# Optimization experiments

Measured on AMD Instinct MI355X. Metric: run time of the kernel, lower is better.

## Reference

```python
import jax, jax.numpy as jnp
import numpy as np

B, T, E, HH, V = 64, 128, 256, 256, 50000  # HH = hidden_size // 2 per LTC level
DT = 1.0


def setup_inputs() -> dict:
    key = jax.random.key(0)
    ks = jax.random.split(key, 12)
    s_in = 1.0 / np.sqrt(E)
    s_rec = 1.0 / np.sqrt(HH)
    tokens = jax.random.randint(ks[0], (B, T), 0, V, dtype=jnp.int32)
    emb = jax.random.normal(ks[1], (V, E), jnp.float32) * 0.02
    W_in0 = jax.random.normal(ks[2], (HH, E), jnp.float32) * s_in
    W_rec0 = jax.random.normal(ks[3], (HH, HH), jnp.float32) * s_rec
    b0 = jnp.zeros((HH,), jnp.float32)
    tau0 = jax.random.uniform(ks[4], (HH,), jnp.float32)
    # NCP sparsity mask: keep prob = 1 - sparsity_level = 0.5
    mask0 = (jax.random.uniform(ks[5], (HH, HH)) > 0.5).astype(jnp.float32)
    W_in1 = jax.random.normal(ks[6], (HH, HH), jnp.float32) * s_rec
    W_rec1 = jax.random.normal(ks[7], (HH, HH), jnp.float32) * s_rec
    b1 = jnp.zeros((HH,), jnp.float32)
    tau1 = jax.random.uniform(ks[8], (HH,), jnp.float32)
    mask1 = (jax.random.uniform(ks[9], (HH, HH)) > 0.5).astype(jnp.float32)
    return {"tokens": tokens, "emb": emb,
            "W_in0": W_in0, "W_rec0": W_rec0, "b0": b0, "tau0": tau0, "mask0": mask0,
            "W_in1": W_in1, "W_rec1": W_rec1, "b1": b1, "tau1": tau1, "mask1": mask1}


def _ltc_scan(x_seq, W_in, W_rec, mask, b, tau_raw):
    """LTC Euler integration over time. x_seq: [B, T, D] -> [B, T, H]."""
    tau = jax.nn.softplus(tau_raw) + 0.1        # positive time constants [H]
    Wr = W_rec * mask                            # NCP sparse recurrent weights
    x_proj = jnp.einsum('btd,hd->bth', x_seq, W_in) + b  # precompute input drive
    h0 = jnp.zeros((x_seq.shape[0], W_rec.shape[0]), x_seq.dtype)

    def step(h, xp_t):
        pre = xp_t + h @ Wr.T
        h_new = h + DT * ((-h + jnp.tanh(pre)) / tau)
        return h_new, h_new

    _, hs = jax.lax.scan(step, h0, jnp.swapaxes(x_proj, 0, 1))  # [T, B, H]
    return jnp.swapaxes(hs, 0, 1)


def reference(tokens, emb, W_in0, W_rec0, b0, tau0, mask0,
              W_in1, W_rec1, b1, tau1, mask1):
    x = emb[tokens]                                   # [B, T, E]
    h0_seq = _ltc_scan(x, W_in0, W_rec0, mask0, b0, tau0)      # level 0: [B, T, HH]
    h1_seq = _ltc_scan(h0_seq, W_in1, W_rec1, mask1, b1, tau1)  # level 1: [B, T, HH]
    return jnp.concatenate([h0_seq, h1_seq], axis=-1)  # [B, T, 2*HH] = hidden_size
```

## Files before the change

### kernel.cpp

```cpp
#include <hip/hip_runtime.h>
#include <hip/hip_bf16.h>

#define B_ 64
#define T_ 128
#define E_ 256
#define H_ 256
#define OW_ 512
#define LP 264
#define MAGIC 0x5AD00000u

typedef unsigned short ushort_t;
typedef __attribute__((ext_vector_type(8))) short bf16x8;
typedef __attribute__((ext_vector_type(4))) float f32x4;

#define LGKM_BARRIER() asm volatile("s_waitcnt lgkmcnt(0)\n\ts_barrier" ::: "memory")

__device__ __forceinline__ ushort_t f2bf(float f) {
    unsigned int x = __float_as_uint(f);
    unsigned int r = x + 0x7FFFu + ((x >> 16) & 1u);
    return (ushort_t)(r >> 16);
}
__device__ __forceinline__ float fast_tanh(float x) {
    float e = __expf(2.0f * x);
    return 1.0f - 2.0f * __builtin_amdgcn_rcpf(e + 1.0f);
}
__device__ __forceinline__ bf16x8 load_bfrag(const float* W, const float* M,
                                             size_t base) {
    float4 a = *(const float4*)(W + base);
    float4 b = *(const float4*)(W + base + 4);
    if (M) {
        float4 ma = *(const float4*)(M + base);
        float4 mb = *(const float4*)(M + base + 4);
        a.x *= ma.x; a.y *= ma.y; a.z *= ma.z; a.w *= ma.w;
        b.x *= mb.x; b.y *= mb.y; b.z *= mb.z; b.w *= mb.w;
    }
    union { bf16x8 v; ushort_t u[8]; } r;
    r.u[0] = f2bf(a.x); r.u[1] = f2bf(a.y); r.u[2] = f2bf(a.z); r.u[3] = f2bf(a.w);
    r.u[4] = f2bf(b.x); r.u[5] = f2bf(b.y); r.u[6] = f2bf(b.z); r.u[7] = f2bf(b.w);
    return r.v;
}

template<bool FUSE, bool WAIT>
__device__ __forceinline__ void scan_core(
    int grp, ushort_t (*hb16)[16][LP],
    const float* xp, int xp_stride, int xp_col,
    float* hout, int out_col,
    const float* Wrec, const float* Wmask, const float* tau_raw,
    const float* Wf, const float* bfv, float* xf,
    unsigned int* flag)
{
    const int tid  = threadIdx.x;
    const int lane = tid & 63;
    const int wv   = tid >> 6;
    const int quad = lane >> 4;
    const int l15  = lane & 15;
    const int n0   = wv * 32;
    const int bg   = grp * 8;

    bf16x8 Bf[2][8];
    #pragma unroll
    for (int tc = 0; tc < 2; ++tc)
        #pragma unroll
        for (int kk = 0; kk < 8; ++kk)
            Bf[tc][kk] = load_bfrag(Wrec, Wmask,
                (size_t)(n0 + tc * 16 + l15) * H_ + kk * 32 + quad * 8);

    bf16x8 Bf2[2][8];
    float  b2[2] = {0.f, 0.f};
    if (FUSE) {
        #pragma unroll
        for (int tc = 0; tc < 2; ++tc) {
            b2[tc] = bfv[n0 + tc * 16 + l15];
            #pragma unroll
            for (int kk = 0; kk < 8; ++kk)
                Bf2[tc][kk] = load_bfrag(Wf, nullptr,
                    (size_t)(n0 + tc * 16 + l15) * H_ + kk * 32 + quad * 8);
        }
    }

    float inv_tau[2], h_prev[2][2];
    float xp_c[2][2], xp_n[2][2], xp_nn[2][2];
    #pragma unroll
    for (int tc = 0; tc < 2; ++tc) {
        inv_tau[tc] = 1.0f / (logf(1.0f + __expf(tau_raw[n0 + tc * 16 + l15])) + 0.1f);
        #pragma unroll
        for (int reg = 0; reg < 2; ++reg) {
            h_prev[tc][reg] = 0.0f;
            xp_c[tc][reg] = xp_n[tc][reg] = xp_nn[tc][reg] = 0.0f;
        }
    }

    if (!WAIT) {
        #pragma unroll
        for (int tc = 0; tc < 2; ++tc)
            #pragma unroll
            for (int reg = 0; reg < 2; ++reg) {
                const int b = bg + quad * 2 + reg;
                const int c = n0 + tc * 16 + l15;
                xp_c[tc][reg] = xp[(size_t)(b * T_ + 0) * xp_stride + xp_col + c];
                xp_n[tc][reg] = xp[(size_t)(b * T_ + 1) * xp_stride + xp_col + c];
            }
    }

    for (int i = tid; i < 2 * 16 * LP / 2; i += 512)
        ((unsigned int*)&hb16[0][0][0])[i] = 0u;
    __syncthreads();

    const int tmax = FUSE ? T_ : (T_ - 1);
    for (int t = 0; t <= tmax; ++t) {
        const int rb = t & 1;

        if (WAIT && t < T_ && (t & 7) == 0) {
            if (tid == 0) {
                const unsigned need = (unsigned)(t >> 3) + 1u;
                for (;;) {
                    unsigned d = __hip_atomic_load(flag, __ATOMIC_ACQUIRE,
                                                   __HIP_MEMORY_SCOPE_AGENT) - MAGIC;
                    if (d >= need && d <= 16u) break;
                    __builtin_amdgcn_s_sleep(2);
                }
            }
            __syncthreads();
            #pragma unroll
            for (int tc = 0; tc < 2; ++tc)
                #pragma unroll
                for (int reg = 0; reg < 2; ++reg) {
                    const int b = bg + quad * 2 + reg;
                    xp_c[tc][reg] = xp[(size_t)(b * T_ + t) * xp_stride + xp_col
                                       + n0 + tc * 16 + l15];
                }
        }

        bf16x8 Af[8];
        #pragma unroll
        for (int kk = 0; kk < 8; ++kk)
            Af[kk] = *(const bf16x8*)&hb16[rb][l15][kk * 32 + quad * 8];

        if (t < T_) {
            if (WAIT) {
                if ((t & 7) != 7 && t + 1 < T_) {
                    #pragma unroll
                    for (int tc = 0; tc < 2; ++tc)
                        #pragma unroll
                        for (int reg = 0; reg < 2; ++reg) {
                            const int b = bg + quad * 2 + reg;
                            xp_n[tc][reg] = xp[(size_t)(b * T_ + t + 1) * xp_stride
                                               + xp_col + n0 + tc * 16 + l15];
                        }
                }
            } else if (t + 2 < T_) {
                #pragma unroll
                for (int tc = 0; tc < 2; ++tc)
                    #pragma unroll
                    for (int reg = 0; reg < 2; ++reg) {
                        const int b = bg + quad * 2 + reg;
                        xp_nn[tc][reg] = xp[(size_t)(b * T_ + t + 2) * xp_stride
                                            + xp_col + n0 + tc * 16 + l15];
                    }
            }

            f32x4 acc[2] = {{0.f,0.f,0.f,0.f},{0.f,0.f,0.f,0.f}};
            #pragma unroll
            for (int kk = 0; kk < 8; ++kk)
                #pragma unroll
                for (int tc = 0; tc < 2; ++tc)
                    acc[tc] = __builtin_amdgcn_mfma_f32_16x16x32_bf16(
                        Af[kk], Bf[tc][kk], acc[tc], 0, 0, 0);

            #pragma unroll
            for (int tc = 0; tc < 2; ++tc) {
                const int c = n0 + tc * 16 + l15;
                #pragma unroll
                for (int reg = 0; reg < 2; ++reg) {
                    const int b = bg + quad * 2 + reg;
                    const float pre = xp_c[tc][reg] + acc[tc][reg];
                    const float hn  = h_prev[tc][reg]
                                    + (fast_tanh(pre) - h_prev[tc][reg]) * inv_tau[tc];
                    h_prev[tc][reg] = hn;
                    hb16[rb ^ 1][quad * 4 + reg][c] = f2bf(hn);
                    hout[(size_t)(b * T_ + t) * OW_ + out_col + c] = hn;
                }
            }
            if (WAIT) {
                if ((t & 7) != 7) {
                    #pragma unroll
                    for (int tc = 0; tc < 2; ++tc)
                        #pragma unroll
                        for (int reg = 0; reg < 2; ++reg)
                            xp_c[tc][reg] = xp_n[tc][reg];
                }
            } else {
                #pragma unroll
                for (int tc = 0; tc < 2; ++tc)
                    #pragma unroll
                    for (int reg = 0; reg < 2; ++reg) {
                        xp_c[tc][reg] = xp_n[tc][reg];
                        xp_n[tc][reg] = xp_nn[tc][reg];
                    }
            }
        }

        if (FUSE && t > 0) {
            f32x4 acc2[2];
            #pragma unroll
            for (int tc = 0; tc < 2; ++tc)
                acc2[tc] = (f32x4){b2[tc], b2[tc], b2[tc], b2[tc]};
            #pragma unroll
            for (int kk = 0; kk < 8; ++kk)
                #pragma unroll
                for (int tc = 0; tc < 2; ++tc)
                    acc2[tc] = __builtin_amdgcn_mfma_f32_16x16x32_bf16(
                        Af[kk], Bf2[tc][kk], acc2[tc], 0, 0, 0);
            #pragma unroll
            for (int tc = 0; tc < 2; ++tc) {
                const int c = n0 + tc * 16 + l15;
                #pragma unroll
                for (int reg = 0; reg < 2; ++reg) {
                    const int b = bg + quad * 2 + reg;
                    __hip_atomic_store(&xf[(size_t)(b * T_ + t - 1) * H_ + c],
                                       acc2[tc][reg],
                                       __ATOMIC_RELAXED, __HIP_MEMORY_SCOPE_AGENT);
                }
            }
        }

        if (FUSE && t > 0 && (t & 7) == 0) {
            __syncthreads();
            if (tid == 0)
                __hip_atomic_store(flag, MAGIC + (unsigned)(t >> 3),
                                   __ATOMIC_RELEASE, __HIP_MEMORY_SCOPE_AGENT);
        } else if (t < tmax) {
            LGKM_BARRIER();
        }
    }
}

__global__ __launch_bounds__(512, 2)
void ltc_dual(float* out,
              const float* __restrict__ Wr0, const float* __restrict__ m0,
              const float* __restrict__ t0,
              const float* __restrict__ Wi1, const float* __restrict__ b1v,
              const float* __restrict__ Wr1, const float* __restrict__ m1,
              const float* __restrict__ t1,
              float* xf, unsigned int* flags)
{
    __shared__ __align__(16) ushort_t hb16[2][16][LP];
    if (blockIdx.x < 8)
        scan_core<true, false>(blockIdx.x, hb16,
                               out, OW_, H_,
                               out, 0,
                               Wr0, m0, t0, Wi1, b1v, xf, flags + blockIdx.x);
    else
        scan_core<false, true>(blockIdx.x - 8, hb16,
                               xf, H_, 0,
                               out, H_,
                               Wr1, m1, t1, nullptr, nullptr, nullptr,
                               flags + blockIdx.x - 8);
}

__global__ __launch_bounds__(512, 2)
void ltc_single(const float* xp, int xp_stride, int xp_col,
                float* hout, int out_col,
                const float* __restrict__ Wr, const float* __restrict__ mk,
                const float* __restrict__ tu)
{
    __shared__ __align__(16) ushort_t hb16[2][16][LP];
    scan_core<false, false>(blockIdx.x, hb16, xp, xp_stride, xp_col,
                            hout, out_col, Wr, mk, tu,
                            nullptr, nullptr, nullptr, nullptr);
}

__global__ __launch_bounds__(512, 2)
void proj_mfma(const float* __restrict__ src, int src_stride, int src_col,
               const int* __restrict__ tok,
               const float* __restrict__ Wi,
               const float* __restrict__ bias,
               float* __restrict__ dst, int dst_stride, int dst_col)
{
    const int tid  = threadIdx.x;
    const int lane = tid & 63;
    const int wv   = tid >> 6;
    const int quad = lane >> 4;
    const int l15  = lane & 15;
    const int n0   = wv * 32;

    __shared__ __align__(16) ushort_t As[32][LP];

    bf16x8 Bf[2][8];
    float  bj[2];
    #pragma unroll
    for (int tc = 0; tc < 2; ++tc) {
        const int n = n0 + tc * 16 + l15;
        bj[tc] = bias[n];
        #pragma unroll
        for (int kk = 0; kk < 8; ++kk)
            Bf[tc][kk] = load_bfrag(Wi, nullptr, (size_t)n * H_ + kk * 32 + quad * 8);
    }

    const int r0 = blockIdx.x * 32;
    {
        const int row = tid >> 4;
        const int seg = tid & 15;
        const size_t sb = (tok ? (size_t)tok[r0 + row] : (size_t)(r0 + row))
                          * src_stride + src_col + seg * 16;
        union { uint4 q[2]; ushort_t u[16]; } p;
        #pragma unroll
        for (int h = 0; h < 2; ++h) {
            float4 f0 = *(const float4*)(src + sb + h * 8);
            float4 f1 = *(const float4*)(src + sb + h * 8 + 4);
            p.u[h*8+0] = f2bf(f0.x); p.u[h*8+1] = f2bf(f0.y);
            p.u[h*8+2] = f2bf(f0.z); p.u[h*8+3] = f2bf(f0.w);
            p.u[h*8+4] = f2bf(f1.x); p.u[h*8+5] = f2bf(f1.y);
            p.u[h*8+6] = f2bf(f1.z); p.u[h*8+7] = f2bf(f1.w);
        }
        *(uint4*)&As[row][seg * 16]     = p.q[0];
        *(uint4*)&As[row][seg * 16 + 8] = p.q[1];
    }
    __syncthreads();

    #pragma unroll
    for (int rt = 0; rt < 2; ++rt) {
        bf16x8 Af[8];
        #pragma unroll
        for (int kk = 0; kk < 8; ++kk)
            Af[kk] = *(const bf16x8*)&As[rt * 16 + l15][kk * 32 + quad * 8];

        f32x4 acc[2] = {{bj[0],bj[0],bj[0],bj[0]}, {bj[1],bj[1],bj[1],bj[1]}};
        #pragma unroll
        for (int kk = 0; kk < 8; ++kk)
            #pragma unroll
            for (int tc = 0; tc < 2; ++tc)
                acc[tc] = __builtin_amdgcn_mfma_f32_16x16x32_bf16(
                    Af[kk], Bf[tc][kk], acc[tc], 0, 0, 0);

        #pragma unroll
        for (int tc = 0; tc < 2; ++tc) {
            const int c = n0 + tc * 16 + l15;
            #pragma unroll
            for (int reg = 0; reg < 4; ++reg) {
                const int r = r0 + rt * 16 + quad * 4 + reg;
                dst[(size_t)r * dst_stride + dst_col + c] = acc[tc][reg];
            }
        }
    }
}

extern "C" void kernel_launch(void* const* d_in, const int* in_sizes, int n_in,
                              void* d_out, int out_size, void* d_ws, size_t ws_size,
                              hipStream_t stream)
{
    const int*   tokens = (const int*)d_in[0];
    const float* emb    = (const float*)d_in[1];
    const float* W_in0  = (const float*)d_in[2];
    const float* W_rec0 = (const float*)d_in[3];
    const float* b0     = (const float*)d_in[4];
    const float* tau0   = (const float*)d_in[5];
    const float* mask0  = (const float*)d_in[6];
    const float* W_in1  = (const float*)d_in[7];
    const float* W_rec1 = (const float*)d_in[8];
    const float* b1     = (const float*)d_in[9];
    const float* tau1   = (const float*)d_in[10];
    const float* mask1  = (const float*)d_in[11];
    float* out = (float*)d_out;
    (void)in_sizes; (void)n_in; (void)out_size;

    const size_t xf_elems = (size_t)B_ * T_ * H_;
    const bool pipelined = ws_size >= xf_elems * sizeof(float) + 64;

    proj_mfma<<<dim3(256), dim3(512), 0, stream>>>(
        emb, E_, 0, tokens, W_in0, b0, out, OW_, H_);

    if (pipelined) {
        float* xf = (float*)d_ws;
        unsigned int* flags = (unsigned int*)((float*)d_ws + xf_elems);
        ltc_dual<<<dim3(16), dim3(512), 0, stream>>>(
            out, W_rec0, mask0, tau0, W_in1, b1, W_rec1, mask1, tau1, xf, flags);
    } else {
        ltc_single<<<dim3(8), dim3(512), 0, stream>>>(
            out, OW_, H_, out, 0, W_rec0, mask0, tau0);
        proj_mfma<<<dim3(256), dim3(512), 0, stream>>>(
            out, OW_, 0, nullptr, W_in1, b1, out, OW_, H_);
        ltc_single<<<dim3(8), dim3(512), 0, stream>>>(
            out, OW_, H_, out, H_, W_rec1, mask1, tau1);
    }
}
```

Before: 277.4 us.

## Use 4 waves with 64 columns each and a fragment-ordered LDS layout for h

The recurrent scan blocks drop from 8 waves of 32 output columns to 4 waves of 64 columns (TC=4). This halves the number of waves taking part in each per-step barrier, and each wave issues more MFMAs per step. The bf16 hidden-state buffer in LDS is stored in an MFMA-A-fragment-swizzled order, so each lane reads its A fragment as a contiguous 16-byte chunk at lane*8. The cost is a larger register footprint (weight fragments doubled, launch bounds 256,1) and fewer waves available to hide latency in each step.

After: 337.7 us. 21.7% more time.

```diff
diff --git a/kernel.cpp b/kernel.cpp
--- a/kernel.cpp
+++ b/kernel.cpp
@@ -7,6 +7,7 @@
 #define H_ 256
 #define OW_ 512
 #define LP 264
+#define TC 4
 #define MAGIC 0x5AD00000u
 
 typedef unsigned short ushort_t;
@@ -40,9 +41,13 @@
     return r.v;
 }
 
+__device__ __forceinline__ int a_off(int r, int k) {
+    return ((k >> 5) << 9) + (((k >> 3) & 3) << 7) + (r << 3) + (k & 7);
+}
+
 template<bool FUSE, bool WAIT>
 __device__ __forceinline__ void scan_core(
-    int grp, ushort_t (*hb16)[16][LP],
+    int grp, ushort_t (*hb)[4096],
     const float* xp, int xp_stride, int xp_col,
     float* hout, int out_col,
     const float* Wrec, const float* Wmask, const float* tau_raw,
@@ -54,22 +59,22 @@
     const int wv   = tid >> 6;
     const int quad = lane >> 4;
     const int l15  = lane & 15;
-    const int n0   = wv * 32;
+    const int n0   = wv * 64;
     const int bg   = grp * 8;
 
-    bf16x8 Bf[2][8];
+    bf16x8 Bf[TC][8];
     #pragma unroll
-    for (int tc = 0; tc < 2; ++tc)
+    for (int tc = 0; tc < TC; ++tc)
         #pragma unroll
         for (int kk = 0; kk < 8; ++kk)
             Bf[tc][kk] = load_bfrag(Wrec, Wmask,
                 (size_t)(n0 + tc * 16 + l15) * H_ + kk * 32 + quad * 8);
 
-    bf16x8 Bf2[2][8];
-    float  b2[2] = {0.f, 0.f};
+    bf16x8 Bf2[TC][8];
+    float  b2[TC];
     if (FUSE) {
         #pragma unroll
-        for (int tc = 0; tc < 2; ++tc) {
+        for (int tc = 0; tc < TC; ++tc) {
             b2[tc] = bfv[n0 + tc * 16 + l15];
             #pragma unroll
             for (int kk = 0; kk < 8; ++kk)
@@ -78,10 +83,10 @@
         }
     }
 
-    float inv_tau[2], h_prev[2][2];
-    float xp_c[2][2], xp_n[2][2], xp_nn[2][2];
+    float inv_tau[TC], h_prev[TC][2];
+    float xp_c[TC][2], xp_n[TC][2], xp_nn[TC][2];
     #pragma unroll
-    for (int tc = 0; tc < 2; ++tc) {
+    for (int tc = 0; tc < TC; ++tc) {
         inv_tau[tc] = 1.0f / (logf(1.0f + __expf(tau_raw[n0 + tc * 16 + l15])) + 0.1f);
         #pragma unroll
         for (int reg = 0; reg < 2; ++reg) {
@@ -90,9 +95,16 @@
         }
     }
 
+    int woff[TC][2];
+    #pragma unroll
+    for (int tc = 0; tc < TC; ++tc)
+        #pragma unroll
+        for (int reg = 0; reg < 2; ++reg)
+            woff[tc][reg] = a_off(quad * 4 + reg, n0 + tc * 16 + l15);
+
     if (!WAIT) {
         #pragma unroll
-        for (int tc = 0; tc < 2; ++tc)
+        for (int tc = 0; tc < TC; ++tc)
             #pragma unroll
             for (int reg = 0; reg < 2; ++reg) {
                 const int b = bg + quad * 2 + reg;
@@ -102,8 +114,8 @@
             }
     }
 
-    for (int i = tid; i < 2 * 16 * LP / 2; i += 512)
-        ((unsigned int*)&hb16[0][0][0])[i] = 0u;
+    for (int i = tid; i < 4096; i += 256)
+        ((unsigned int*)&hb[0][0])[i] = 0u;
     __syncthreads();
 
     const int tmax = FUSE ? T_ : (T_ - 1);
@@ -122,7 +134,7 @@
             }
             __syncthreads();
             #pragma unroll
-            for (int tc = 0; tc < 2; ++tc)
+            for (int tc = 0; tc < TC; ++tc)
                 #pragma unroll
                 for (int reg = 0; reg < 2; ++reg) {
                     const int b = bg + quad * 2 + reg;
@@ -132,15 +144,18 @@
         }
 
         bf16x8 Af[8];
-        #pragma unroll
-        for (int kk = 0; kk < 8; ++kk)
-            Af[kk] = *(const bf16x8*)&hb16[rb][l15][kk * 32 + quad * 8];
+        {
+            const ushort_t* abase = &hb[rb][lane * 8];
+            #pragma unroll
+            for (int kk = 0; kk < 8; ++kk)
+                Af[kk] = *(const bf16x8*)(abase + kk * 512);
+        }
 
         if (t < T_) {
             if (WAIT) {
                 if ((t & 7) != 7 && t + 1 < T_) {
                     #pragma unroll
-                    for (int tc = 0; tc < 2; ++tc)
+                    for (int tc = 0; tc < TC; ++tc)
                         #pragma unroll
                         for (int reg = 0; reg < 2; ++reg) {
                             const int b = bg + quad * 2 + reg;
@@ -150,7 +165,7 @@
                 }
             } else if (t + 2 < T_) {
                 #pragma unroll
-                for (int tc = 0; tc < 2; ++tc)
+                for (int tc = 0; tc < TC; ++tc)
                     #pragma unroll
                     for (int reg = 0; reg < 2; ++reg) {
                         const int b = bg + quad * 2 + reg;
@@ -159,16 +174,17 @@
                     }
             }
 
-            f32x4 acc[2] = {{0.f,0.f,0.f,0.f},{0.f,0.f,0.f,0.f}};
+            f32x4 acc[TC] = {{0.f,0.f,0.f,0.f},{0.f,0.f,0.f,0.f},
+                             {0.f,0.f,0.f,0.f},{0.f,0.f,0.f,0.f}};
             #pragma unroll
             for (int kk = 0; kk < 8; ++kk)
                 #pragma unroll
-                for (int tc = 0; tc < 2; ++tc)
+                for (int tc = 0; tc < TC; ++tc)
                     acc[tc] = __builtin_amdgcn_mfma_f32_16x16x32_bf16(
                         Af[kk], Bf[tc][kk], acc[tc], 0, 0, 0);
 
             #pragma unroll
-            for (int tc = 0; tc < 2; ++tc) {
+            for (int tc = 0; tc < TC; ++tc) {
                 const int c = n0 + tc * 16 + l15;
                 #pragma unroll
                 for (int reg = 0; reg < 2; ++reg) {
@@ -177,21 +193,21 @@
                     const float hn  = h_prev[tc][reg]
                                     + (fast_tanh(pre) - h_prev[tc][reg]) * inv_tau[tc];
                     h_prev[tc][reg] = hn;
-                    hb16[rb ^ 1][quad * 4 + reg][c] = f2bf(hn);
+                    hb[rb ^ 1][woff[tc][reg]] = f2bf(hn);
                     hout[(size_t)(b * T_ + t) * OW_ + out_col + c] = hn;
                 }
             }
             if (WAIT) {
                 if ((t & 7) != 7) {
                     #pragma unroll
-                    for (int tc = 0; tc < 2; ++tc)
+                    for (int tc = 0; tc < TC; ++tc)
                         #pragma unroll
                         for (int reg = 0; reg < 2; ++reg)
                             xp_c[tc][reg] = xp_n[tc][reg];
                 }
             } else {
                 #pragma unroll
-                for (int tc = 0; tc < 2; ++tc)
+                for (int tc = 0; tc < TC; ++tc)
                     #pragma unroll
                     for (int reg = 0; reg < 2; ++reg) {
                         xp_c[tc][reg] = xp_n[tc][reg];
@@ -201,18 +217,18 @@
         }
 
         if (FUSE && t > 0) {
-            f32x4 acc2[2];
-            #pragma unroll
-            for (int tc = 0; tc < 2; ++tc)
+            f32x4 acc2[TC];
+            #pragma unroll
+            for (int tc = 0; tc < TC; ++tc)
                 acc2[tc] = (f32x4){b2[tc], b2[tc], b2[tc], b2[tc]};
             #pragma unroll
             for (int kk = 0; kk < 8; ++kk)
                 #pragma unroll
-                for (int tc = 0; tc < 2; ++tc)
+                for (int tc = 0; tc < TC; ++tc)
                     acc2[tc] = __builtin_amdgcn_mfma_f32_16x16x32_bf16(
                         Af[kk], Bf2[tc][kk], acc2[tc], 0, 0, 0);
             #pragma unroll
-            for (int tc = 0; tc < 2; ++tc) {
+            for (int tc = 0; tc < TC; ++tc) {
                 const int c = n0 + tc * 16 + l15;
                 #pragma unroll
                 for (int reg = 0; reg < 2; ++reg) {
@@ -235,7 +251,7 @@
     }
 }
 
-__global__ __launch_bounds__(512, 2)
+__global__ __launch_bounds__(256, 1)
 void ltc_dual(float* out,
               const float* __restrict__ Wr0, const float* __restrict__ m0,
               const float* __restrict__ t0,
@@ -244,28 +260,28 @@
               const float* __restrict__ t1,
               float* xf, unsigned int* flags)
 {
-    __shared__ __align__(16) ushort_t hb16[2][16][LP];
+    __shared__ __align__(16) ushort_t hb[2][4096];
     if (blockIdx.x < 8)
-        scan_core<true, false>(blockIdx.x, hb16,
+        scan_core<true, false>(blockIdx.x, hb,
                                out, OW_, H_,
                                out, 0,
                                Wr0, m0, t0, Wi1, b1v, xf, flags + blockIdx.x);
     else
-        scan_core<false, true>(blockIdx.x - 8, hb16,
+        scan_core<false, true>(blockIdx.x - 8, hb,
                                xf, H_, 0,
                                out, H_,
                                Wr1, m1, t1, nullptr, nullptr, nullptr,
                                flags + blockIdx.x - 8);
 }
 
-__global__ __launch_bounds__(512, 2)
+__global__ __launch_bounds__(256, 1)
 void ltc_single(const float* xp, int xp_stride, int xp_col,
                 float* hout, int out_col,
                 const float* __restrict__ Wr, const float* __restrict__ mk,
                 const float* __restrict__ tu)
 {
-    __shared__ __align__(16) ushort_t hb16[2][16][LP];
-    scan_core<false, false>(blockIdx.x, hb16, xp, xp_stride, xp_col,
+    __shared__ __align__(16) ushort_t hb[2][4096];
+    scan_core<false, false>(blockIdx.x, hb, xp, xp_stride, xp_col,
                             hout, out_col, Wr, mk, tu,
                             nullptr, nullptr, nullptr, nullptr);
 }
@@ -373,14 +389,14 @@
     if (pipelined) {
         float* xf = (float*)d_ws;
         unsigned int* flags = (unsigned int*)((float*)d_ws + xf_elems);
-        ltc_dual<<<dim3(16), dim3(512), 0, stream>>>(
+        ltc_dual<<<dim3(16), dim3(256), 0, stream>>>(
             out, W_rec0, mask0, tau0, W_in1, b1, W_rec1, mask1, tau1, xf, flags);
     } else {
-        ltc_single<<<dim3(8), dim3(512), 0, stream>>>(
+        ltc_single<<<dim3(8), dim3(256), 0, stream>>>(
             out, OW_, H_, out, 0, W_rec0, mask0, tau0);
         proj_mfma<<<dim3(256), dim3(512), 0, stream>>>(
             out, OW_, 0, nullptr, W_in1, b1, out, OW_, H_);
-        ltc_single<<<dim3(8), dim3(512), 0, stream>>>(
+        ltc_single<<<dim3(8), dim3(256), 0, stream>>>(
             out, OW_, H_, out, H_, W_rec1, mask1, tau1);
     }
 }
```

## Merge both LTC levels into one skewed per-block scan with prepacked weight fragments

Applied to the files above, without the earlier changes.

Replaces the producer/consumer two-block-group pipeline, which used flag polling and a global xf buffer, with a single kernel. Each block runs the level-0 step t and the level-1 step t-1 together, so the level-1 input projection is computed on-chip and the cross-block synchronization goes away. A new pack kernel converts the masked recurrent and input weights to bf16 MFMA fragments in the workspace. Two of the three weight sets are re-read from global/L2 every timestep to limit register pressure. The LDS h-buffer layout is changed to a fragment-ordered swizzle, and the fallback path uses 256-thread blocks.

Measured after the change: 495.3 us. 1.79x slower.

```diff
diff --git a/kernel.cpp b/kernel.cpp
--- a/kernel.cpp
+++ b/kernel.cpp
@@ -40,14 +40,33 @@
     return r.v;
 }
 
-template<bool FUSE, bool WAIT>
-__device__ __forceinline__ void scan_core(
-    int grp, ushort_t (*hb16)[16][LP],
-    const float* xp, int xp_stride, int xp_col,
-    float* hout, int out_col,
-    const float* Wrec, const float* Wmask, const float* tau_raw,
-    const float* Wf, const float* bfv, float* xf,
-    unsigned int* flag)
+__device__ __forceinline__ int a_off(int r, int k) {
+    return ((k >> 5) << 9) + (((k >> 3) & 3) << 7) + (r << 3) + (k & 7);
+}
+
+__global__ __launch_bounds__(64, 8)
+void pack_frags(const float* __restrict__ Wr0, const float* __restrict__ m0,
+                const float* __restrict__ Wi1,
+                const float* __restrict__ Wr1, const float* __restrict__ m1,
+                bf16x8* __restrict__ pk)
+{
+    const int mat  = blockIdx.x >> 7;
+    const int f    = blockIdx.x & 127;
+    const int lane = threadIdx.x;
+    const int wv = f >> 4, tc2 = (f >> 3) & 1, kk = f & 7;
+    const int quad = lane >> 4, l15 = lane & 15;
+    const int c = wv * 32 + tc2 * 16 + l15;
+    const size_t base = (size_t)c * H_ + kk * 32 + quad * 8;
+    const float* W = (mat == 0) ? Wr0 : (mat == 1) ? Wi1 : Wr1;
+    const float* M = (mat == 0) ? m0  : (mat == 1) ? nullptr : m1;
+    pk[(size_t)blockIdx.x * 64 + lane] = load_bfrag(W, M, base);
+}
+
+__global__ __launch_bounds__(512, 2)
+void ltc_merged(float* out, const bf16x8* __restrict__ pk,
+                const float* __restrict__ tau0,
+                const float* __restrict__ b1v,
+                const float* __restrict__ tau1)
 {
     const int tid  = threadIdx.x;
     const int lane = tid & 63;
@@ -55,33 +74,203 @@
     const int quad = lane >> 4;
     const int l15  = lane & 15;
     const int n0   = wv * 32;
+    const int bg   = blockIdx.x * 8;
+    const bool rlane = (l15 & 2) == 0;
+
+    __shared__ __align__(16) ushort_t hb[2][2][4096];
+
+    const bf16x8* pk0 = pk + (size_t)(wv * 16) * 64;
+    const bf16x8* pk1 = pk + (size_t)(128 + wv * 16) * 64;
+    const bf16x8* pk2 = pk + (size_t)(256 + wv * 16) * 64;
+
+    bf16x8 Bf0[2][8];
+    #pragma unroll
+    for (int tc = 0; tc < 2; ++tc)
+        #pragma unroll
+        for (int kk = 0; kk < 8; ++kk)
+            Bf0[tc][kk] = pk0[(tc * 8 + kk) * 64 + lane];
+
+    float inv_t0[2], inv_t1[2], b2[2], h0p[2][2], h1p[2][2];
+    #pragma unroll
+    for (int tc = 0; tc < 2; ++tc) {
+        const int c = n0 + tc * 16 + l15;
+        inv_t0[tc] = 1.0f / (logf(1.0f + __expf(tau0[c])) + 0.1f);
+        inv_t1[tc] = 1.0f / (logf(1.0f + __expf(tau1[c])) + 0.1f);
+        b2[tc] = b1v[c];
+        h0p[tc][0] = h0p[tc][1] = 0.f;
+        h1p[tc][0] = h1p[tc][1] = 0.f;
+    }
+
+    int woff[2][2];
+    #pragma unroll
+    for (int tc = 0; tc < 2; ++tc)
+        #pragma unroll
+        for (int reg = 0; reg < 2; ++reg)
+            woff[tc][reg] = a_off(quad * 4 + reg, n0 + tc * 16 + l15);
+
+    float xp_c[2][2], xp_n[2][2];
+    #pragma unroll
+    for (int tc = 0; tc < 2; ++tc)
+        #pragma unroll
+        for (int reg = 0; reg < 2; ++reg) {
+            const int b = bg + quad * 2 + reg;
+            xp_c[tc][reg] = out[(size_t)(b * T_) * OW_ + H_ + n0 + tc * 16 + l15];
+            xp_n[tc][reg] = 0.f;
+        }
+
+    for (int i = tid; i < 2 * 2 * 4096 / 2; i += 512)
+        ((unsigned int*)&hb[0][0][0])[i] = 0u;
+
+    const int ab = rlane ? (lane * 8) : 0;
+
+    __syncthreads();
+
+    #pragma unroll 1
+    for (int t = 0; t <= T_; ++t) {
+        const int rb = t & 1;
+        bf16x8 Bs[2][8];
+
+        #pragma unroll
+        for (int tc = 0; tc < 2; ++tc)
+            #pragma unroll
+            for (int kk = 0; kk < 8; ++kk)
+                Bs[tc][kk] = pk1[(tc * 8 + kk) * 64 + lane];
+
+        if (t + 1 < T_) {
+            #pragma unroll
+            for (int tc = 0; tc < 2; ++tc)
+                #pragma unroll
+                for (int reg = 0; reg < 2; ++reg) {
+                    const int b = bg + quad * 2 + reg;
+                    xp_n[tc][reg] = out[(size_t)(b * T_ + t + 1) * OW_ + H_
+                                        + n0 + tc * 16 + l15];
+                }
+        }
+
+        bf16x8 Af0[8];
+        {
+            const ushort_t* a0 = &hb[0][rb][0];
+            #pragma unroll
+            for (int kk = 0; kk < 8; ++kk)
+                Af0[kk] = *(const bf16x8*)(a0 + ab + kk * 512);
+        }
+
+        f32x4 acc0[2] = {{0.f,0.f,0.f,0.f},{0.f,0.f,0.f,0.f}};
+        if (t < T_) {
+            #pragma unroll
+            for (int kk = 0; kk < 8; ++kk)
+                #pragma unroll
+                for (int tc = 0; tc < 2; ++tc)
+                    acc0[tc] = __builtin_amdgcn_mfma_f32_16x16x32_bf16(
+                        Af0[kk], Bf0[tc][kk], acc0[tc], 0, 0, 0);
+        }
+
+        f32x4 acc2[2];
+        if (t > 0) {
+            #pragma unroll
+            for (int tc = 0; tc < 2; ++tc)
+                acc2[tc] = (f32x4){b2[tc], b2[tc], b2[tc], b2[tc]};
+            #pragma unroll
+            for (int kk = 0; kk < 8; ++kk)
+                #pragma unroll
+                for (int tc = 0; tc < 2; ++tc)
+                    acc2[tc] = __builtin_amdgcn_mfma_f32_16x16x32_bf16(
+                        Af0[kk], Bs[tc][kk], acc2[tc], 0, 0, 0);
+        }
+
+        #pragma unroll
+        for (int tc = 0; tc < 2; ++tc)
+            #pragma unroll
+            for (int kk = 0; kk < 8; ++kk)
+                Bs[tc][kk] = pk2[(tc * 8 + kk) * 64 + lane];
+
+        bf16x8 Af1[8];
+        {
+            const ushort_t* a1 = &hb[1][rb][0];
+            #pragma unroll
+            for (int kk = 0; kk < 8; ++kk)
+                Af1[kk] = *(const bf16x8*)(a1 + ab + kk * 512);
+        }
+
+        if (t < T_) {
+            #pragma unroll
+            for (int tc = 0; tc < 2; ++tc) {
+                const int c = n0 + tc * 16 + l15;
+                #pragma unroll
+                for (int reg = 0; reg < 2; ++reg) {
+                    const int b = bg + quad * 2 + reg;
+                    const float pre = xp_c[tc][reg] + acc0[tc][reg];
+                    const float hn  = h0p[tc][reg]
+                                    + (fast_tanh(pre) - h0p[tc][reg]) * inv_t0[tc];
+                    h0p[tc][reg] = hn;
+                    hb[0][rb ^ 1][woff[tc][reg]] = f2bf(hn);
+                    out[(size_t)(b * T_ + t) * OW_ + c] = hn;
+                }
+            }
+            #pragma unroll
+            for (int tc = 0; tc < 2; ++tc)
+                #pragma unroll
+                for (int reg = 0; reg < 2; ++reg)
+                    xp_c[tc][reg] = xp_n[tc][reg];
+        }
+
+        if (t > 0) {
+            f32x4 acc1[2] = {{0.f,0.f,0.f,0.f},{0.f,0.f,0.f,0.f}};
+            #pragma unroll
+            for (int kk = 0; kk < 8; ++kk)
+                #pragma unroll
+                for (int tc = 0; tc < 2; ++tc)
+                    acc1[tc] = __builtin_amdgcn_mfma_f32_16x16x32_bf16(
+                        Af1[kk], Bs[tc][kk], acc1[tc], 0, 0, 0);
+            #pragma unroll
+            for (int tc = 0; tc < 2; ++tc) {
+                const int c = n0 + tc * 16 + l15;
+                #pragma unroll
+                for (int reg = 0; reg < 2; ++reg) {
+                    const int b = bg + quad * 2 + reg;
+                    const float pre = acc2[tc][reg] + acc1[tc][reg];
+                    const float hn  = h1p[tc][reg]
+                                    + (fast_tanh(pre) - h1p[tc][reg]) * inv_t1[tc];
+                    h1p[tc][reg] = hn;
+                    hb[1][rb ^ 1][woff[tc][reg]] = f2bf(hn);
+                    out[(size_t)(b * T_ + t - 1) * OW_ + H_ + c] = hn;
+                }
+            }
+        }
+
+        if (t < T_) LGKM_BARRIER();
+    }
+}
+
+template<bool FUSE, bool WAIT>
+__device__ __forceinline__ void scan_core(
+    int grp, ushort_t (*hb)[4096],
+    const float* xp, int xp_stride, int xp_col,
+    float* hout, int out_col,
+    const float* Wrec, const float* Wmask, const float* tau_raw,
+    const float* Wf, const float* bfv, float* xf,
+    unsigned int* flag)
+{
+    const int tid  = threadIdx.x;
+    const int lane = tid & 63;
+    const int wv   = tid >> 6;
+    const int quad = lane >> 4;
+    const int l15  = lane & 15;
+    const int n0   = wv * 64;
     const int bg   = grp * 8;
 
-    bf16x8 Bf[2][8];
-    #pragma unroll
-    for (int tc = 0; tc < 2; ++tc)
+    bf16x8 Bf[4][8];
+    #pragma unroll
+    for (int tc = 0; tc < 4; ++tc)
         #pragma unroll
         for (int kk = 0; kk < 8; ++kk)
             Bf[tc][kk] = load_bfrag(Wrec, Wmask,
                 (size_t)(n0 + tc * 16 + l15) * H_ + kk * 32 + quad * 8);
 
-    bf16x8 Bf2[2][8];
-    float  b2[2] = {0.f, 0.f};
-    if (FUSE) {
-        #pragma unroll
-        for (int tc = 0; tc < 2; ++tc) {
-            b2[tc] = bfv[n0 + tc * 16 + l15];
-            #pragma unroll
-            for (int kk = 0; kk < 8; ++kk)
-                Bf2[tc][kk] = load_bfrag(Wf, nullptr,
-                    (size_t)(n0 + tc * 16 + l15) * H_ + kk * 32 + quad * 8);
-        }
-    }
-
-    float inv_tau[2], h_prev[2][2];
-    float xp_c[2][2], xp_n[2][2], xp_nn[2][2];
-    #pragma unroll
-    for (int tc = 0; tc < 2; ++tc) {
+    float inv_tau[4], h_prev[4][2];
+    float xp_c[4][2], xp_n[4][2], xp_nn[4][2];
+    #pragma unroll
+    for (int tc = 0; tc < 4; ++tc) {
         inv_tau[tc] = 1.0f / (logf(1.0f + __expf(tau_raw[n0 + tc * 16 + l15])) + 0.1f);
         #pragma unroll
         for (int reg = 0; reg < 2; ++reg) {
@@ -90,182 +279,92 @@
         }
     }
 
-    if (!WAIT) {
-        #pragma unroll
-        for (int tc = 0; tc < 2; ++tc)
+    int woff[4][2];
+    #pragma unroll
+    for (int tc = 0; tc < 4; ++tc)
+        #pragma unroll
+        for (int reg = 0; reg < 2; ++reg)
+            woff[tc][reg] = a_off(quad * 4 + reg, n0 + tc * 16 + l15);
+
+    #pragma unroll
+    for (int tc = 0; tc < 4; ++tc)
+        #pragma unroll
+        for (int reg = 0; reg < 2; ++reg) {
+            const int b = bg + quad * 2 + reg;
+            const int c = n0 + tc * 16 + l15;
+            xp_c[tc][reg] = xp[(size_t)(b * T_ + 0) * xp_stride + xp_col + c];
+            xp_n[tc][reg] = xp[(size_t)(b * T_ + 1) * xp_stride + xp_col + c];
+        }
+
+    for (int i = tid; i < 4096; i += 256)
+        ((unsigned int*)&hb[0][0])[i] = 0u;
+    __syncthreads();
+
+    for (int t = 0; t < T_; ++t) {
+        const int rb = t & 1;
+
+        bf16x8 Af[8];
+        {
+            const ushort_t* abase = &hb[rb][lane * 8];
+            #pragma unroll
+            for (int kk = 0; kk < 8; ++kk)
+                Af[kk] = *(const bf16x8*)(abase + kk * 512);
+        }
+
+        if (t + 2 < T_) {
+            #pragma unroll
+            for (int tc = 0; tc < 4; ++tc)
+                #pragma unroll
+                for (int reg = 0; reg < 2; ++reg) {
+                    const int b = bg + quad * 2 + reg;
+                    xp_nn[tc][reg] = xp[(size_t)(b * T_ + t + 2) * xp_stride
+                                        + xp_col + n0 + tc * 16 + l15];
+                }
+        }
+
+        f32x4 acc[4] = {{0.f,0.f,0.f,0.f},{0.f,0.f,0.f,0.f},
+                        {0.f,0.f,0.f,0.f},{0.f,0.f,0.f,0.f}};
+        #pragma unroll
+        for (int kk = 0; kk < 8; ++kk)
+            #pragma unroll
+            for (int tc = 0; tc < 4; ++tc)
+                acc[tc] = __builtin_amdgcn_mfma_f32_16x16x32_bf16(
+                    Af[kk], Bf[tc][kk], acc[tc], 0, 0, 0);
+
+        #pragma unroll
+        for (int tc = 0; tc < 4; ++tc) {
+            const int c = n0 + tc * 16 + l15;
             #pragma unroll
             for (int reg = 0; reg < 2; ++reg) {
                 const int b = bg + quad * 2 + reg;
-                const int c = n0 + tc * 16 + l15;
-                xp_c[tc][reg] = xp[(size_t)(b * T_ + 0) * xp_stride + xp_col + c];
-                xp_n[tc][reg] = xp[(size_t)(b * T_ + 1) * xp_stride + xp_col + c];
+                const float pre = xp_c[tc][reg] + acc[tc][reg];
+                const float hn  = h_prev[tc][reg]
+                                + (fast_tanh(pre) - h_prev[tc][reg]) * inv_tau[tc];
+                h_prev[tc][reg] = hn;
+                hb[rb ^ 1][woff[tc][reg]] = f2bf(hn);
+                hout[(size_t)(b * T_ + t) * OW_ + out_col + c] = hn;
             }
-    }
-
-    for (int i = tid; i < 2 * 16 * LP / 2; i += 512)
-        ((unsigned int*)&hb16[0][0][0])[i] = 0u;
-    __syncthreads();
-
-    const int tmax = FUSE ? T_ : (T_ - 1);
-    for (int t = 0; t <= tmax; ++t) {
-        const int rb = t & 1;
-
-        if (WAIT && t < T_ && (t & 7) == 0) {
-            if (tid == 0) {
-                const unsigned need = (unsigned)(t >> 3) + 1u;
-                for (;;) {
-                    unsigned d = __hip_atomic_load(flag, __ATOMIC_ACQUIRE,
-                                                   __HIP_MEMORY_SCOPE_AGENT) - MAGIC;
-                    if (d >= need && d <= 16u) break;
-                    __builtin_amdgcn_s_sleep(2);
-                }
+        }
+        #pragma unroll
+        for (int tc = 0; tc < 4; ++tc)
+            #pragma unroll
+            for (int reg = 0; reg < 2; ++reg) {
+                xp_c[tc][reg] = xp_n[tc][reg];
+                xp_n[tc][reg] = xp_nn[tc][reg];
             }
-            __syncthreads();
-            #pragma unroll
-            for (int tc = 0; tc < 2; ++tc)
-                #pragma unroll
-                for (int reg = 0; reg < 2; ++reg) {
-                    const int b = bg + quad * 2 + reg;
-                    xp_c[tc][reg] = xp[(size_t)(b * T_ + t) * xp_stride + xp_col
-                                       + n0 + tc * 16 + l15];
-                }
-        }
-
-        bf16x8 Af[8];
-        #pragma unroll
-        for (int kk = 0; kk < 8; ++kk)
-            Af[kk] = *(const bf16x8*)&hb16[rb][l15][kk * 32 + quad * 8];
-
-        if (t < T_) {
-            if (WAIT) {
-                if ((t & 7) != 7 && t + 1 < T_) {
-                    #pragma unroll
-                    for (int tc = 0; tc < 2; ++tc)
-                        #pragma unroll
-                        for (int reg = 0; reg < 2; ++reg) {
-                            const int b = bg + quad * 2 + reg;
-                            xp_n[tc][reg] = xp[(size_t)(b * T_ + t + 1) * xp_stride
-                                               + xp_col + n0 + tc * 16 + l15];
-                        }
-                }
-            } else if (t + 2 < T_) {
-                #pragma unroll
-                for (int tc = 0; tc < 2; ++tc)
-                    #pragma unroll
-                    for (int reg = 0; reg < 2; ++reg) {
-                        const int b = bg + quad * 2 + reg;
-                        xp_nn[tc][reg] = xp[(size_t)(b * T_ + t + 2) * xp_stride
-                                            + xp_col + n0 + tc * 16 + l15];
-                    }
-            }
-
-            f32x4 acc[2] = {{0.f,0.f,0.f,0.f},{0.f,0.f,0.f,0.f}};
-            #pragma unroll
-            for (int kk = 0; kk < 8; ++kk)
-                #pragma unroll
-                for (int tc = 0; tc < 2; ++tc)
-                    acc[tc] = __builtin_amdgcn_mfma_f32_16x16x32_bf16(
-                        Af[kk], Bf[tc][kk], acc[tc], 0, 0, 0);
-
-            #pragma unroll
-            for (int tc = 0; tc < 2; ++tc) {
-                const int c = n0 + tc * 16 + l15;
-                #pragma unroll
-                for (int reg = 0; reg < 2; ++reg) {
-                    const int b = bg + quad * 2 + reg;
-                    const float pre = xp_c[tc][reg] + acc[tc][reg];
-                    const float hn  = h_prev[tc][reg]
-                                    + (fast_tanh(pre) - h_prev[tc][reg]) * inv_tau[tc];
-                    h_prev[tc][reg] = hn;
-                    hb16[rb ^ 1][quad * 4 + reg][c] = f2bf(hn);
-                    hout[(size_t)(b * T_ + t) * OW_ + out_col + c] = hn;
-                }
-            }
-            if (WAIT) {
-                if ((t & 7) != 7) {
-                    #pragma unroll
-                    for (int tc = 0; tc < 2; ++tc)
-                        #pragma unroll
-                        for (int reg = 0; reg < 2; ++reg)
-                            xp_c[tc][reg] = xp_n[tc][reg];
-                }
-            } else {
-                #pragma unroll
-                for (int tc = 0; tc < 2; ++tc)
-                    #pragma unroll
-                    for (int reg = 0; reg < 2; ++reg) {
-                        xp_c[tc][reg] = xp_n[tc][reg];
-                        xp_n[tc][reg] = xp_nn[tc][reg];
-                    }
-            }
-        }
-
-        if (FUSE && t > 0) {
-            f32x4 acc2[2];
-            #pragma unroll
-            for (int tc = 0; tc < 2; ++tc)
-                acc2[tc] = (f32x4){b2[tc], b2[tc], b2[tc], b2[tc]};
-            #pragma unroll
-            for (int kk = 0; kk < 8; ++kk)
-                #pragma unroll
-                for (int tc = 0; tc < 2; ++tc)
-                    acc2[tc] = __builtin_amdgcn_mfma_f32_16x16x32_bf16(
-                        Af[kk], Bf2[tc][kk], acc2[tc], 0, 0, 0);
-            #pragma unroll
-            for (int tc = 0; tc < 2; ++tc) {
-                const int c = n0 + tc * 16 + l15;
-                #pragma unroll
-                for (int reg = 0; reg < 2; ++reg) {
-                    const int b = bg + quad * 2 + reg;
-                    __hip_atomic_store(&xf[(size_t)(b * T_ + t - 1) * H_ + c],
-                                       acc2[tc][reg],
-                                       __ATOMIC_RELAXED, __HIP_MEMORY_SCOPE_AGENT);
-                }
-            }
-        }
-
-        if (FUSE && t > 0 && (t & 7) == 0) {
-            __syncthreads();
-            if (tid == 0)
-                __hip_atomic_store(flag, MAGIC + (unsigned)(t >> 3),
-                                   __ATOMIC_RELEASE, __HIP_MEMORY_SCOPE_AGENT);
-        } else if (t < tmax) {
-            LGKM_BARRIER();
-        }
-    }
-}
-
-__global__ __launch_bounds__(512, 2)
-void ltc_dual(float* out,
-              const float* __restrict__ Wr0, const float* __restrict__ m0,
-              const float* __restrict__ t0,
-              const float* __restrict__ Wi1, const float* __restrict__ b1v,
-              const float* __restrict__ Wr1, const float* __restrict__ m1,
-              const float* __restrict__ t1,
-              float* xf, unsigned int* flags)
-{
-    __shared__ __align__(16) ushort_t hb16[2][16][LP];
-    if (blockIdx.x < 8)
-        scan_core<true, false>(blockIdx.x, hb16,
-                               out, OW_, H_,
-                               out, 0,
-                               Wr0, m0, t0, Wi1, b1v, xf, flags + blockIdx.x);
-    else
-        scan_core<false, true>(blockIdx.x - 8, hb16,
-                               xf, H_, 0,
-                               out, H_,
-                               Wr1, m1, t1, nullptr, nullptr, nullptr,
-                               flags + blockIdx.x - 8);
-}
-
-__global__ __launch_bounds__(512, 2)
+
+        if (t + 1 < T_) LGKM_BARRIER();
+    }
+}
+
+__global__ __launch_bounds__(256, 1)
 void ltc_single(const float* xp, int xp_stride, int xp_col,
                 float* hout, int out_col,
                 const float* __restrict__ Wr, const float* __restrict__ mk,
                 const float* __restrict__ tu)
 {
-    __shared__ __align__(16) ushort_t hb16[2][16][LP];
-    scan_core<false, false>(blockIdx.x, hb16, xp, xp_stride, xp_col,
+    __shared__ __align__(16) ushort_t hb[2][4096];
+    scan_core<false, false>(blockIdx.x, hb, xp, xp_stride, xp_col,
                             hout, out_col, Wr, mk, tu,
                             nullptr, nullptr, nullptr, nullptr);
 }
@@ -364,23 +463,24 @@
     float* out = (float*)d_out;
     (void)in_sizes; (void)n_in; (void)out_size;
 
-    const size_t xf_elems = (size_t)B_ * T_ * H_;
-    const bool pipelined = ws_size >= xf_elems * sizeof(float) + 64;
-
-    proj_mfma<<<dim3(256), dim3(512), 0, stream>>>(
-        emb, E_, 0, tokens, W_in0, b0, out, OW_, H_);
-
-    if (pipelined) {
-        float* xf = (float*)d_ws;
-        unsigned int* flags = (unsigned int*)((float*)d_ws + xf_elems);
-        ltc_dual<<<dim3(16), dim3(512), 0, stream>>>(
-            out, W_rec0, mask0, tau0, W_in1, b1, W_rec1, mask1, tau1, xf, flags);
+    const size_t pk_bytes = (size_t)3 * 128 * 64 * 16;
+
+    if (ws_size >= pk_bytes) {
+        bf16x8* pk = (bf16x8*)d_ws;
+        pack_frags<<<dim3(384), dim3(64), 0, stream>>>(
+            W_rec0, mask0, W_in1, W_rec1, mask1, pk);
+        proj_mfma<<<dim3(256), dim3(512), 0, stream>>>(
+            emb, E_, 0, tokens, W_in0, b0, out, OW_, H_);
+        ltc_merged<<<dim3(8), dim3(512), 0, stream>>>(
+            out, pk, tau0, b1, tau1);
     } else {
-        ltc_single<<<dim3(8), dim3(512), 0, stream>>>(
+        proj_mfma<<<dim3(256), dim3(512), 0, stream>>>(
+            emb, E_, 0, tokens, W_in0, b0, out, OW_, H_);
+        ltc_single<<<dim3(8), dim3(256), 0, stream>>>(
             out, OW_, H_, out, 0, W_rec0, mask0, tau0);
         proj_mfma<<<dim3(256), dim3(512), 0, stream>>>(
             out, OW_, 0, nullptr, W_in1, b1, out, OW_, H_);
-        ltc_single<<<dim3(8), dim3(512), 0, stream>>>(
+        ltc_single<<<dim3(8), dim3(256), 0, stream>>>(
             out, OW_, H_, out, H_, W_rec1, mask1, tau1);
     }
 }
```
